# Kernel tuning notes

Hardware: AMD Instinct MI355X
Metric: run time of the kernel (lower is better)

## Reference

```python
import jax, jax.numpy as jnp
import numpy as np

N = 50000      # nodes
E = 800000     # edges (avg degree 16)
IN = 512       # in_feats
HID = 64       # hidden_dim
HEADS = 4      # num_heads
NC = 40        # num_classes


def setup_inputs() -> dict:
    key = jax.random.key(0)
    ks = jax.random.split(key, 12)

    def p(k, shape, fan_in):
        return jax.random.normal(k, shape, jnp.float32) * (1.0 / np.sqrt(fan_in))

    x = jax.random.normal(ks[0], (N, IN), jnp.float32)
    edge_index = jax.random.randint(ks[1], (2, E), 0, N)
    return dict(
        x=x,
        edge_index=edge_index,
        W1=p(ks[2], (IN, HEADS * HID), IN),
        att_src1=p(ks[3], (HEADS, HID), HID),
        att_dst1=p(ks[4], (HEADS, HID), HID),
        b1=jnp.zeros((HEADS * HID,), jnp.float32),
        W2=p(ks[5], (HEADS * HID, HID), HEADS * HID),
        att_src2=p(ks[6], (1, HID), HID),
        att_dst2=p(ks[7], (1, HID), HID),
        b2=jnp.zeros((HID,), jnp.float32),
        mw1=p(ks[8], (HID, 64), HID),
        mb1=jnp.zeros((64,), jnp.float32),
        mw2=p(ks[9], (64, NC), 64),
        mb2=jnp.zeros((NC,), jnp.float32),
    )


def gat_layer(x, edge_index, W, att_src, att_dst, bias):
    # PyG GATConv with add_self_loops=False, concat=True, negative_slope=0.2
    H, C = att_src.shape
    n = x.shape[0]
    h = (x @ W).reshape(n, H, C)                       # [N,H,C]
    a_src = jnp.sum(h * att_src, axis=-1)              # [N,H]
    a_dst = jnp.sum(h * att_dst, axis=-1)              # [N,H]
    src, dst = edge_index[0], edge_index[1]
    e = jax.nn.leaky_relu(a_src[src] + a_dst[dst], 0.2)  # [E,H]
    # segment softmax grouped by destination node
    m = jax.ops.segment_max(e, dst, num_segments=n)
    ex = jnp.exp(e - m[dst])
    denom = jax.ops.segment_sum(ex, dst, num_segments=n)
    alpha = ex / (denom[dst] + 1e-16)                  # [E,H]
    out = jax.ops.segment_sum(h[src] * alpha[:, :, None], dst, num_segments=n)  # [N,H,C]
    return out.reshape(n, H * C) + bias


def reference(x, edge_index, W1, att_src1, att_dst1, b1,
              W2, att_src2, att_dst2, b2, mw1, mb1, mw2, mb2):
    h = jax.nn.elu(gat_layer(x, edge_index, W1, att_src1, att_dst1, b1))   # [N, HEADS*HID]
    emb = gat_layer(h, edge_index, W2, att_src2, att_dst2, b2)             # [N, HID] (heads=1)
    return jax.nn.relu(emb @ mw1 + mb1) @ mw2 + mb2                        # [N, NC]
```

## Files before the change

### kernel.cpp

```cpp
#include <hip/hip_runtime.h>

#define N_NODES 50000
#define N_EDGES 800000
#define SCAN_B 196

typedef short bf16x8 __attribute__((ext_vector_type(8)));
typedef float f32x4 __attribute__((ext_vector_type(4)));

#define GLDS16(g, l)                                                  \
  __builtin_amdgcn_global_load_lds(                                   \
      (const __attribute__((address_space(1))) void*)(g),             \
      (__attribute__((address_space(3))) void*)(l), 16, 0, 0)

__device__ __forceinline__ unsigned short f2bf_rne(float x) {
  unsigned u = __float_as_uint(x);
  u += 0x7FFFu + ((u >> 16) & 1u);
  return (unsigned short)(u >> 16);
}

__device__ __forceinline__ void split2(float x, short& hi, short& lo) {
  unsigned u = __float_as_uint(x);
  unsigned short h = (unsigned short)(u >> 16);
  float hf = __uint_as_float((unsigned)h << 16);
  float r = x - hf;
  unsigned short l = (unsigned short)(__float_as_uint(r) >> 16);
  hi = (short)h;
  lo = (short)l;
}

__global__ __launch_bounds__(256) void hist_k(const int* __restrict__ ei,
                                              int* __restrict__ cnt) {
  int e = blockIdx.x * 256 + threadIdx.x;
  if (e >= N_EDGES) return;
  atomicAdd(&cnt[ei[N_EDGES + e]], 1);
}

__global__ __launch_bounds__(256) void scan1(const int* __restrict__ cnt,
                                             int* __restrict__ offs,
                                             int* __restrict__ bsum) {
  __shared__ int sh[256];
  int t = threadIdx.x;
  int i = blockIdx.x * 256 + t;
  int v = (i < N_NODES) ? cnt[i] : 0;
  sh[t] = v;
  __syncthreads();
  for (int off = 1; off < 256; off <<= 1) {
    int add = (t >= off) ? sh[t - off] : 0;
    __syncthreads();
    sh[t] += add;
    __syncthreads();
  }
  if (i < N_NODES) offs[i] = sh[t] - v;
  if (t == 255) bsum[blockIdx.x] = sh[255];
}

__global__ __launch_bounds__(256) void scan2(const int* __restrict__ bsum,
                                             int* __restrict__ bofs) {
  __shared__ int sh[256];
  int t = threadIdx.x;
  int v = (t < SCAN_B) ? bsum[t] : 0;
  sh[t] = v;
  __syncthreads();
  for (int off = 1; off < 256; off <<= 1) {
    int add = (t >= off) ? sh[t - off] : 0;
    __syncthreads();
    sh[t] += add;
    __syncthreads();
  }
  if (t < SCAN_B) bofs[t] = sh[t] - v;
}

__global__ __launch_bounds__(256) void scan3(int* __restrict__ offs,
                                             const int* __restrict__ bofs) {
  int i = blockIdx.x * 256 + threadIdx.x;
  if (i < N_NODES) offs[i] += bofs[blockIdx.x];
  if (i == 0) offs[N_NODES] = N_EDGES;
}

__global__ __launch_bounds__(256) void scatter_k(const int* __restrict__ ei,
                                                 const int* __restrict__ offs,
                                                 int* __restrict__ cur,
                                                 int* __restrict__ ssort) {
  int e = blockIdx.x * 256 + threadIdx.x;
  if (e >= N_EDGES) return;
  int d = ei[N_EDGES + e];
  int p = offs[d] + atomicAdd(&cur[d], 1);
  ssort[p] = ei[e];
}

__global__ __launch_bounds__(256) void wsplit(
    const float* __restrict__ W, unsigned short* __restrict__ Wh,
    unsigned short* __restrict__ Wl, int K, int Nn) {
  int i = blockIdx.x * 256 + threadIdx.x;
  int total = (K >> 3) * Nn;
  if (i >= total) return;
  int kq = i / Nn;
  int n = i % Nn;
  alignas(16) short h[8], l[8];
#pragma unroll
  for (int j = 0; j < 8; ++j) {
    float v = W[(size_t)(kq * 8 + j) * Nn + n];
    split2(v, h[j], l[j]);
  }
  size_t dst = (size_t)i * 8;
  *(bf16x8*)&Wh[dst] = *(bf16x8*)h;
  *(bf16x8*)&Wl[dst] = *(bf16x8*)l;
}

__global__ __launch_bounds__(256) void gemm1_fused(
    const float* __restrict__ A,
    const unsigned short* __restrict__ Bh_g, const unsigned short* __restrict__ Bl_g,
    const float* __restrict__ att_s, const float* __restrict__ att_d,
    unsigned short* __restrict__ h1b, float* __restrict__ asrc,
    float* __restrict__ adst, int M) {
  constexpr int K = 512, Nn = 256;
  constexpr int LDA = 40;
  __shared__ short Ah[128][LDA], Al[128][LDA];
  __shared__ short Bh[4 * 128 * 8], Bl[4 * 128 * 8];
  __shared__ float attLds[128][4];

  const int tid = threadIdx.x;
  const int wave = tid >> 6, lane = tid & 63;
  const int quad = lane >> 4, l16 = lane & 15;
  const int wm = (wave >> 1) * 64, wn = (wave & 1) * 64;
  const int rowBase = blockIdx.x * 128;
  const int colBase = blockIdx.y * 128;

  const int ra = tid >> 1, apart = (tid & 1) * 16;
  const int arow = min(rowBase + ra, M - 1);
  const float* aptr = A + (size_t)arow * K + apart;

  f32x4 acc[4][4] = {};

  for (int kc = 0; kc < K / 32; ++kc) {
#pragma unroll
    for (int inst = 0; inst < 2; ++inst) {
      int seq = inst * 256 + tid;
      int gq = seq >> 7, nl = seq & 127;
      size_t gsrc = (((size_t)kc * 4 + gq) * Nn + colBase + nl) * 8;
      GLDS16(Bh_g + gsrc, &Bh[seq * 8]);
      GLDS16(Bl_g + gsrc, &Bl[seq * 8]);
    }
    {
      alignas(16) short h[16], l[16];
      const float4* a4 = (const float4*)(aptr + kc * 32);
#pragma unroll
      for (int i = 0; i < 4; ++i) {
        float4 v = a4[i];
        split2(v.x, h[i * 4 + 0], l[i * 4 + 0]);
        split2(v.y, h[i * 4 + 1], l[i * 4 + 1]);
        split2(v.z, h[i * 4 + 2], l[i * 4 + 2]);
        split2(v.w, h[i * 4 + 3], l[i * 4 + 3]);
      }
      *(bf16x8*)&Ah[ra][apart]     = ((bf16x8*)h)[0];
      *(bf16x8*)&Ah[ra][apart + 8] = ((bf16x8*)h)[1];
      *(bf16x8*)&Al[ra][apart]     = ((bf16x8*)l)[0];
      *(bf16x8*)&Al[ra][apart + 8] = ((bf16x8*)l)[1];
    }
    __syncthreads();
    bf16x8 afh[4], afl[4], bfh[4], bfl[4];
#pragma unroll
    for (int mt = 0; mt < 4; ++mt) {
      afh[mt] = *(const bf16x8*)&Ah[wm + mt * 16 + l16][quad * 8];
      afl[mt] = *(const bf16x8*)&Al[wm + mt * 16 + l16][quad * 8];
    }
#pragma unroll
    for (int nt = 0; nt < 4; ++nt) {
      int bi = ((quad << 7) + wn + nt * 16 + l16) * 8;
      bfh[nt] = *(const bf16x8*)&Bh[bi];
      bfl[nt] = *(const bf16x8*)&Bl[bi];
    }
#pragma unroll
    for (int mt = 0; mt < 4; ++mt)
#pragma unroll
      for (int nt = 0; nt < 4; ++nt) {
        acc[mt][nt] = __builtin_amdgcn_mfma_f32_16x16x32_bf16(afh[mt], bfh[nt], acc[mt][nt], 0, 0, 0);
        acc[mt][nt] = __builtin_amdgcn_mfma_f32_16x16x32_bf16(afh[mt], bfl[nt], acc[mt][nt], 0, 0, 0);
        acc[mt][nt] = __builtin_amdgcn_mfma_f32_16x16x32_bf16(afl[mt], bfh[nt], acc[mt][nt], 0, 0, 0);
      }
    __syncthreads();
  }

  float asw[4], adw[4];
#pragma unroll
  for (int nt = 0; nt < 4; ++nt) {
    int c = colBase + wn + nt * 16 + l16;
    asw[nt] = att_s[c];
    adw[nt] = att_d[c];
  }
#pragma unroll
  for (int mt = 0; mt < 4; ++mt) {
    int rl = wm + mt * 16 + quad * 4;
#pragma unroll
    for (int reg = 0; reg < 4; ++reg) {
      int r = rowBase + rl + reg;
      float s = 0.f, dd = 0.f;
#pragma unroll
      for (int nt = 0; nt < 4; ++nt) {
        float v = acc[mt][nt][reg];
        s += v * asw[nt];
        dd += v * adw[nt];
        if (r < M) {
          int c = colBase + wn + nt * 16 + l16;
          h1b[(size_t)r * Nn + c] = f2bf_rne(v);
        }
      }
#pragma unroll
      for (int off = 1; off < 16; off <<= 1) {
        s += __shfl_xor(s, off);
        dd += __shfl_xor(dd, off);
      }
      if (l16 == 0) {
        attLds[rl + reg][(wn >> 6) * 2 + 0] = s;
        attLds[rl + reg][(wn >> 6) * 2 + 1] = dd;
      }
    }
  }
  __syncthreads();
  if (tid < 128) {
    int r = rowBase + tid;
    if (r < M) {
      int hb = colBase >> 6;
      asrc[r * 4 + hb + 0] = attLds[tid][0];
      adst[r * 4 + hb + 0] = attLds[tid][1];
      asrc[r * 4 + hb + 1] = attLds[tid][2];
      adst[r * 4 + hb + 1] = attLds[tid][3];
    }
  }
}

__global__ __launch_bounds__(256) void gemm2_fused(
    const float* __restrict__ A,
    const unsigned short* __restrict__ Bh_g, const unsigned short* __restrict__ Bl_g,
    const float* __restrict__ att_s, const float* __restrict__ att_d,
    unsigned short* __restrict__ h2b, float* __restrict__ asrc,
    float* __restrict__ adst, int M) {
  constexpr int K = 256, Nn = 64;
  constexpr int LDA = 40;
  __shared__ short Ah[128][LDA], Al[128][LDA];
  __shared__ short Bh[4 * 64 * 8], Bl[4 * 64 * 8];
  __shared__ float attLds[128][2];

  const int tid = threadIdx.x;
  const int wave = tid >> 6, lane = tid & 63;
  const int quad = lane >> 4, l16 = lane & 15;
  const int wm = wave * 32;
  const int rowBase = blockIdx.x * 128;

  const int ra = tid >> 1, apart = (tid & 1) * 16;
  const int arow = min(rowBase + ra, M - 1);
  const float* aptr = A + (size_t)arow * K + apart;

  f32x4 acc[2][4] = {};

  for (int kc = 0; kc < K / 32; ++kc) {
    {
      size_t gsrc = (((size_t)kc * 4) * Nn) * 8 + (size_t)tid * 8;
      GLDS16(Bh_g + gsrc, &Bh[tid * 8]);
      GLDS16(Bl_g + gsrc, &Bl[tid * 8]);
    }
    {
      alignas(16) short h[16], l[16];
      const float4* a4 = (const float4*)(aptr + kc * 32);
#pragma unroll
      for (int i = 0; i < 4; ++i) {
        float4 v = a4[i];
        split2(v.x, h[i * 4 + 0], l[i * 4 + 0]);
        split2(v.y, h[i * 4 + 1], l[i * 4 + 1]);
        split2(v.z, h[i * 4 + 2], l[i * 4 + 2]);
        split2(v.w, h[i * 4 + 3], l[i * 4 + 3]);
      }
      *(bf16x8*)&Ah[ra][apart]     = ((bf16x8*)h)[0];
      *(bf16x8*)&Ah[ra][apart + 8] = ((bf16x8*)h)[1];
      *(bf16x8*)&Al[ra][apart]     = ((bf16x8*)l)[0];
      *(bf16x8*)&Al[ra][apart + 8] = ((bf16x8*)l)[1];
    }
    __syncthreads();
    bf16x8 afh[2], afl[2], bfh[4], bfl[4];
#pragma unroll
    for (int mt = 0; mt < 2; ++mt) {
      afh[mt] = *(const bf16x8*)&Ah[wm + mt * 16 + l16][quad * 8];
      afl[mt] = *(const bf16x8*)&Al[wm + mt * 16 + l16][quad * 8];
    }
#pragma unroll
    for (int nt = 0; nt < 4; ++nt) {
      int bi = ((quad << 6) + nt * 16 + l16) * 8;
      bfh[nt] = *(const bf16x8*)&Bh[bi];
      bfl[nt] = *(const bf16x8*)&Bl[bi];
    }
#pragma unroll
    for (int mt = 0; mt < 2; ++mt)
#pragma unroll
      for (int nt = 0; nt < 4; ++nt) {
        acc[mt][nt] = __builtin_amdgcn_mfma_f32_16x16x32_bf16(afh[mt], bfh[nt], acc[mt][nt], 0, 0, 0);
        acc[mt][nt] = __builtin_amdgcn_mfma_f32_16x16x32_bf16(afh[mt], bfl[nt], acc[mt][nt], 0, 0, 0);
        acc[mt][nt] = __builtin_amdgcn_mfma_f32_16x16x32_bf16(afl[mt], bfh[nt], acc[mt][nt], 0, 0, 0);
      }
    __syncthreads();
  }

  float asw[4], adw[4];
#pragma unroll
  for (int nt = 0; nt < 4; ++nt) {
    int c = nt * 16 + l16;
    asw[nt] = att_s[c];
    adw[nt] = att_d[c];
  }
#pragma unroll
  for (int mt = 0; mt < 2; ++mt) {
    int rl = wm + mt * 16 + quad * 4;
#pragma unroll
    for (int reg = 0; reg < 4; ++reg) {
      int r = rowBase + rl + reg;
      float s = 0.f, dd = 0.f;
#pragma unroll
      for (int nt = 0; nt < 4; ++nt) {
        float v = acc[mt][nt][reg];
        s += v * asw[nt];
        dd += v * adw[nt];
        if (r < M) {
          int c = nt * 16 + l16;
          h2b[(size_t)r * Nn + c] = f2bf_rne(v);
        }
      }
#pragma unroll
      for (int off = 1; off < 16; off <<= 1) {
        s += __shfl_xor(s, off);
        dd += __shfl_xor(dd, off);
      }
      if (l16 == 0) {
        attLds[rl + reg][0] = s;
        attLds[rl + reg][1] = dd;
      }
    }
  }
  __syncthreads();
  if (tid < 128) {
    int r = rowBase + tid;
    if (r < M) {
      asrc[r] = attLds[tid][0];
      adst[r] = attLds[tid][1];
    }
  }
}

__global__ __launch_bounds__(128) void agg_l1(
    const int* __restrict__ offs, const int* __restrict__ ssort,
    const float* __restrict__ asrc, const float* __restrict__ adst,
    const unsigned short* __restrict__ h1b, const float* __restrict__ b1,
    float* __restrict__ outp) {
  const int d = blockIdx.x;
  const int t = threadIdx.x;
  const int h = t >> 5;
  __shared__ int s_src[128];
  __shared__ float s_ex[128 * 4];
  const int row0 = offs[d], row1 = offs[d + 1];
  const float4 ad4 = *(const float4*)&adst[d * 4];
  float acc0 = 0.f, acc1 = 0.f, denom = 0.f;

  for (int j0 = row0; j0 < row1; j0 += 128) {
    const int n = min(128, row1 - j0);
    if (t < n) {
      int s = ssort[j0 + t];
      s_src[t] = s;
      float4 as = *(const float4*)&asrc[s * 4];
      float4 sc;
      sc.x = as.x + ad4.x; sc.x = sc.x > 0.f ? sc.x : 0.2f * sc.x;
      sc.y = as.y + ad4.y; sc.y = sc.y > 0.f ? sc.y : 0.2f * sc.y;
      sc.z = as.z + ad4.z; sc.z = sc.z > 0.f ? sc.z : 0.2f * sc.z;
      sc.w = as.w + ad4.w; sc.w = sc.w > 0.f ? sc.w : 0.2f * sc.w;
      sc.x = __expf(sc.x); sc.y = __expf(sc.y);
      sc.z = __expf(sc.z); sc.w = __expf(sc.w);
      *(float4*)&s_ex[t * 4] = sc;
    }
    __syncthreads();
    for (int j = 0; j < n; ++j) {
      float exv = s_ex[j * 4 + h];
      unsigned pv = *(const unsigned*)&h1b[(size_t)s_src[j] * 256 + 2 * t];
      float f0 = __uint_as_float(pv << 16);
      float f1 = __uint_as_float(pv & 0xFFFF0000u);
      acc0 += f0 * exv;
      acc1 += f1 * exv;
      denom += exv;
    }
    __syncthreads();
  }
  float inv = denom > 0.f ? 1.f / denom : 0.f;
  float v0 = acc0 * inv + b1[2 * t];
  float v1 = acc1 * inv + b1[2 * t + 1];
  float2 r;
  r.x = v0 > 0.f ? v0 : expm1f(v0);
  r.y = v1 > 0.f ? v1 : expm1f(v1);
  *(float2*)&outp[(size_t)d * 256 + 2 * t] = r;
}

__global__ __launch_bounds__(256) void agg_l2(
    const int* __restrict__ offs, const int* __restrict__ ssort,
    const float* __restrict__ asrc, const float* __restrict__ adst,
    const unsigned short* __restrict__ h2b, const float* __restrict__ b2,
    float* __restrict__ outp, int n_nodes) {
  int d = blockIdx.x * 4 + (threadIdx.x >> 6);
  int lane = threadIdx.x & 63;
  if (d >= n_nodes) return;
  const int row0 = offs[d], row1 = offs[d + 1];
  const float ad = adst[d];
  float acc = 0.f, denom = 0.f;

  for (int j0 = row0; j0 < row1; j0 += 64) {
    const int n = min(64, row1 - j0);
    int s = 0;
    float ex = 0.f;
    if (lane < n) {
      s = ssort[j0 + lane];
      float sc = asrc[s] + ad;
      sc = sc > 0.f ? sc : 0.2f * sc;
      ex = __expf(sc);
    }
    float ds = ex;
#pragma unroll
    for (int off = 32; off > 0; off >>= 1) ds += __shfl_xor(ds, off);
    denom += ds;
    for (int j = 0; j < n; ++j) {
      int sj = __shfl(s, j);
      float exj = __shfl(ex, j);
      float f = __uint_as_float((unsigned)h2b[(size_t)sj * 64 + lane] << 16);
      acc += f * exj;
    }
  }
  float val = (denom > 0.f ? acc / denom : 0.f) + b2[lane];
  outp[(size_t)d * 64 + lane] = val;
}

__global__ __launch_bounds__(256) void mlp_head(
    const float* __restrict__ emb_in,
    const float* __restrict__ mw1, const float* __restrict__ mb1,
    const float* __restrict__ mw2, const float* __restrict__ mb2,
    float* __restrict__ outp, int n) {
  __shared__ float w1s[64 * 64];
  __shared__ float w2s[64 * 40];
  __shared__ float b1s[64];
  __shared__ float b2s[40];
  int t = threadIdx.x;
  for (int i = t; i < 64 * 64; i += 256) w1s[i] = mw1[i];
  for (int i = t; i < 64 * 40; i += 256) w2s[i] = mw2[i];
  if (t < 64) b1s[t] = mb1[t];
  if (t < 40) b2s[t] = mb2[t];
  __syncthreads();
  int node = blockIdx.x * 256 + t;
  if (node >= n) return;
  float emb[64];
#pragma unroll
  for (int i = 0; i < 64; ++i) emb[i] = emb_in[(size_t)node * 64 + i];
  float hid[64];
#pragma unroll
  for (int j = 0; j < 64; ++j) {
    float s = b1s[j];
#pragma unroll
    for (int i = 0; i < 64; ++i) s += emb[i] * w1s[i * 64 + j];
    hid[j] = s > 0.f ? s : 0.f;
  }
#pragma unroll
  for (int k = 0; k < 40; ++k) {
    float s = b2s[k];
#pragma unroll
    for (int j = 0; j < 64; ++j) s += hid[j] * w2s[j * 40 + k];
    outp[(size_t)node * 40 + k] = s;
  }
}

extern "C" void kernel_launch(void* const* d_in, const int* in_sizes, int n_in,
                              void* d_out, int out_size, void* d_ws, size_t ws_size,
                              hipStream_t stream) {
  const float* x        = (const float*)d_in[0];
  const int*   ei       = (const int*)d_in[1];
  const float* W1       = (const float*)d_in[2];
  const float* att_src1 = (const float*)d_in[3];
  const float* att_dst1 = (const float*)d_in[4];
  const float* b1       = (const float*)d_in[5];
  const float* W2       = (const float*)d_in[6];
  const float* att_src2 = (const float*)d_in[7];
  const float* att_dst2 = (const float*)d_in[8];
  const float* b2       = (const float*)d_in[9];
  const float* mw1      = (const float*)d_in[10];
  const float* mb1      = (const float*)d_in[11];
  const float* mw2      = (const float*)d_in[12];
  const float* mb2      = (const float*)d_in[13];
  float* out = (float*)d_out;

  const int N = N_NODES, E = N_EDGES;
  char* base = (char*)d_ws;
  size_t o = 0;
  auto alloc = [&](size_t n_elems) {
    void* p = base + o;
    o += n_elems * 4;
    return p;
  };
  int* cnt = (int*)alloc(N);
  int* cur = (int*)alloc(N);
  size_t zero_bytes = o;
  int*   offs  = (int*)alloc(N + 2);
  int*   bsum  = (int*)alloc(256);
  int*   bofs  = (int*)alloc(256);
  int*   ssort = (int*)alloc(E);
  float* h1e   = (float*)alloc((size_t)N * 256);
  float* asrc1 = (float*)alloc((size_t)N * 4);
  float* adst1 = (float*)alloc((size_t)N * 4);
  float* emb   = (float*)alloc((size_t)N * 64);
  float* asrc2 = (float*)alloc(N);
  float* adst2 = (float*)alloc(N);
  unsigned short* h1b = (unsigned short*)alloc((size_t)N * 128);
  unsigned short* h2b = (unsigned short*)alloc((size_t)N * 32);
  unsigned short* w1h = (unsigned short*)alloc(512 * 256 / 2);
  unsigned short* w1l = (unsigned short*)alloc(512 * 256 / 2);
  unsigned short* w2h = (unsigned short*)alloc(256 * 64 / 2);
  unsigned short* w2l = (unsigned short*)alloc(256 * 64 / 2);

  hipMemsetAsync(d_ws, 0, zero_bytes, stream);

  const int EB = (E + 255) / 256;

  hist_k<<<EB, 256, 0, stream>>>(ei, cnt);
  scan1<<<SCAN_B, 256, 0, stream>>>(cnt, offs, bsum);
  scan2<<<1, 256, 0, stream>>>(bsum, bofs);
  scan3<<<SCAN_B, 256, 0, stream>>>(offs, bofs);
  scatter_k<<<EB, 256, 0, stream>>>(ei, offs, cur, ssort);
  wsplit<<<(512 / 8 * 256 + 255) / 256, 256, 0, stream>>>(W1, w1h, w1l, 512, 256);
  wsplit<<<(256 / 8 * 64 + 255) / 256, 256, 0, stream>>>(W2, w2h, w2l, 256, 64);

  dim3 g1((N + 127) / 128, 2);
  gemm1_fused<<<g1, 256, 0, stream>>>(x, w1h, w1l, att_src1, att_dst1,
                                      h1b, asrc1, adst1, N);
  agg_l1<<<N, 128, 0, stream>>>(offs, ssort, asrc1, adst1, h1b, b1, h1e);

  dim3 g2((N + 127) / 128, 1);
  gemm2_fused<<<g2, 256, 0, stream>>>(h1e, w2h, w2l, att_src2, att_dst2,
                                      h2b, asrc2, adst2, N);
  agg_l2<<<(N + 3) / 4, 256, 0, stream>>>(offs, ssort, asrc2, adst2, h2b, b2, emb, N);

  mlp_head<<<(N + 255) / 256, 256, 0, stream>>>(emb, mw1, mb1, mw2, mb2, out, N);
}
```

Before: 514.8 us.

## Double-buffer LDS tiles in both GEMM kernels to overlap loads with MFMA

```diff
diff --git a/kernel.cpp b/kernel.cpp
--- a/kernel.cpp
+++ b/kernel.cpp
@@ -113,10 +113,10 @@
     const float* __restrict__ att_s, const float* __restrict__ att_d,
     unsigned short* __restrict__ h1b, float* __restrict__ asrc,
     float* __restrict__ adst, int M) {
-  constexpr int K = 512, Nn = 256;
+  constexpr int K = 512, Nn = 256, NKC = K / 32;
   constexpr int LDA = 40;
-  __shared__ short Ah[128][LDA], Al[128][LDA];
-  __shared__ short Bh[4 * 128 * 8], Bl[4 * 128 * 8];
+  __shared__ short Ah[2][128][LDA], Al[2][128][LDA];
+  __shared__ short Bh[2][4 * 128 * 8], Bl[2][4 * 128 * 8];
   __shared__ float attLds[128][4];
 
   const int tid = threadIdx.x;
@@ -132,43 +132,60 @@
 
   f32x4 acc[4][4] = {};
 
-  for (int kc = 0; kc < K / 32; ++kc) {
-#pragma unroll
-    for (int inst = 0; inst < 2; ++inst) {
-      int seq = inst * 256 + tid;
-      int gq = seq >> 7, nl = seq & 127;
-      size_t gsrc = (((size_t)kc * 4 + gq) * Nn + colBase + nl) * 8;
-      GLDS16(Bh_g + gsrc, &Bh[seq * 8]);
-      GLDS16(Bl_g + gsrc, &Bl[seq * 8]);
-    }
-    {
-      alignas(16) short h[16], l[16];
-      const float4* a4 = (const float4*)(aptr + kc * 32);
-#pragma unroll
-      for (int i = 0; i < 4; ++i) {
-        float4 v = a4[i];
-        split2(v.x, h[i * 4 + 0], l[i * 4 + 0]);
-        split2(v.y, h[i * 4 + 1], l[i * 4 + 1]);
-        split2(v.z, h[i * 4 + 2], l[i * 4 + 2]);
-        split2(v.w, h[i * 4 + 3], l[i * 4 + 3]);
-      }
-      *(bf16x8*)&Ah[ra][apart]     = ((bf16x8*)h)[0];
-      *(bf16x8*)&Ah[ra][apart + 8] = ((bf16x8*)h)[1];
-      *(bf16x8*)&Al[ra][apart]     = ((bf16x8*)l)[0];
-      *(bf16x8*)&Al[ra][apart + 8] = ((bf16x8*)l)[1];
-    }
-    __syncthreads();
+#pragma unroll
+  for (int inst = 0; inst < 2; ++inst) {
+    int seq = inst * 256 + tid;
+    int gq = seq >> 7, nl = seq & 127;
+    size_t gsrc = (((size_t)gq) * Nn + colBase + nl) * 8;
+    GLDS16(Bh_g + gsrc, &Bh[0][seq * 8]);
+    GLDS16(Bl_g + gsrc, &Bl[0][seq * 8]);
+  }
+  {
+    alignas(16) short h[16], l[16];
+    const float4* a4 = (const float4*)(aptr);
+#pragma unroll
+    for (int i = 0; i < 4; ++i) {
+      float4 v = a4[i];
+      split2(v.x, h[i * 4 + 0], l[i * 4 + 0]);
+      split2(v.y, h[i * 4 + 1], l[i * 4 + 1]);
+      split2(v.z, h[i * 4 + 2], l[i * 4 + 2]);
+      split2(v.w, h[i * 4 + 3], l[i * 4 + 3]);
+    }
+    *(bf16x8*)&Ah[0][ra][apart]     = ((bf16x8*)h)[0];
+    *(bf16x8*)&Ah[0][ra][apart + 8] = ((bf16x8*)h)[1];
+    *(bf16x8*)&Al[0][ra][apart]     = ((bf16x8*)l)[0];
+    *(bf16x8*)&Al[0][ra][apart + 8] = ((bf16x8*)l)[1];
+  }
+  __syncthreads();
+
+  for (int kc = 0; kc < NKC; ++kc) {
+    const int cur = kc & 1, nxt = cur ^ 1;
+    const bool hasNext = (kc + 1 < NKC);
+    float4 av[4];
+    if (hasNext) {
+#pragma unroll
+      for (int inst = 0; inst < 2; ++inst) {
+        int seq = inst * 256 + tid;
+        int gq = seq >> 7, nl = seq & 127;
+        size_t gsrc = (((size_t)(kc + 1) * 4 + gq) * Nn + colBase + nl) * 8;
+        GLDS16(Bh_g + gsrc, &Bh[nxt][seq * 8]);
+        GLDS16(Bl_g + gsrc, &Bl[nxt][seq * 8]);
+      }
+      const float4* a4 = (const float4*)(aptr + (kc + 1) * 32);
+#pragma unroll
+      for (int i = 0; i < 4; ++i) av[i] = a4[i];
+    }
     bf16x8 afh[4], afl[4], bfh[4], bfl[4];
 #pragma unroll
     for (int mt = 0; mt < 4; ++mt) {
-      afh[mt] = *(const bf16x8*)&Ah[wm + mt * 16 + l16][quad * 8];
-      afl[mt] = *(const bf16x8*)&Al[wm + mt * 16 + l16][quad * 8];
+      afh[mt] = *(const bf16x8*)&Ah[cur][wm + mt * 16 + l16][quad * 8];
+      afl[mt] = *(const bf16x8*)&Al[cur][wm + mt * 16 + l16][quad * 8];
     }
 #pragma unroll
     for (int nt = 0; nt < 4; ++nt) {
       int bi = ((quad << 7) + wn + nt * 16 + l16) * 8;
-      bfh[nt] = *(const bf16x8*)&Bh[bi];
-      bfl[nt] = *(const bf16x8*)&Bl[bi];
+      bfh[nt] = *(const bf16x8*)&Bh[cur][bi];
+      bfl[nt] = *(const bf16x8*)&Bl[cur][bi];
     }
 #pragma unroll
     for (int mt = 0; mt < 4; ++mt)
@@ -178,6 +195,21 @@
         acc[mt][nt] = __builtin_amdgcn_mfma_f32_16x16x32_bf16(afh[mt], bfl[nt], acc[mt][nt], 0, 0, 0);
         acc[mt][nt] = __builtin_amdgcn_mfma_f32_16x16x32_bf16(afl[mt], bfh[nt], acc[mt][nt], 0, 0, 0);
       }
+    __builtin_amdgcn_sched_barrier(0);
+    if (hasNext) {
+      alignas(16) short h[16], l[16];
+#pragma unroll
+      for (int i = 0; i < 4; ++i) {
+        split2(av[i].x, h[i * 4 + 0], l[i * 4 + 0]);
+        split2(av[i].y, h[i * 4 + 1], l[i * 4 + 1]);
+        split2(av[i].z, h[i * 4 + 2], l[i * 4 + 2]);
+        split2(av[i].w, h[i * 4 + 3], l[i * 4 + 3]);
+      }
+      *(bf16x8*)&Ah[nxt][ra][apart]     = ((bf16x8*)h)[0];
+      *(bf16x8*)&Ah[nxt][ra][apart + 8] = ((bf16x8*)h)[1];
+      *(bf16x8*)&Al[nxt][ra][apart]     = ((bf16x8*)l)[0];
+      *(bf16x8*)&Al[nxt][ra][apart + 8] = ((bf16x8*)l)[1];
+    }
     __syncthreads();
   }
 
@@ -235,10 +267,10 @@
     const float* __restrict__ att_s, const float* __restrict__ att_d,
     unsigned short* __restrict__ h2b, float* __restrict__ asrc,
     float* __restrict__ adst, int M) {
-  constexpr int K = 256, Nn = 64;
+  constexpr int K = 256, Nn = 64, NKC = K / 32;
   constexpr int LDA = 40;
-  __shared__ short Ah[128][LDA], Al[128][LDA];
-  __shared__ short Bh[4 * 64 * 8], Bl[4 * 64 * 8];
+  __shared__ short Ah[2][128][LDA], Al[2][128][LDA];
+  __shared__ short Bh[2][4 * 64 * 8], Bl[2][4 * 64 * 8];
   __shared__ float attLds[128][2];
 
   const int tid = threadIdx.x;
@@ -253,40 +285,54 @@
 
   f32x4 acc[2][4] = {};
 
-  for (int kc = 0; kc < K / 32; ++kc) {
-    {
-      size_t gsrc = (((size_t)kc * 4) * Nn) * 8 + (size_t)tid * 8;
-      GLDS16(Bh_g + gsrc, &Bh[tid * 8]);
-      GLDS16(Bl_g + gsrc, &Bl[tid * 8]);
-    }
-    {
-      alignas(16) short h[16], l[16];
-      const float4* a4 = (const float4*)(aptr + kc * 32);
-#pragma unroll
-      for (int i = 0; i < 4; ++i) {
-        float4 v = a4[i];
-        split2(v.x, h[i * 4 + 0], l[i * 4 + 0]);
-        split2(v.y, h[i * 4 + 1], l[i * 4 + 1]);
-        split2(v.z, h[i * 4 + 2], l[i * 4 + 2]);
-        split2(v.w, h[i * 4 + 3], l[i * 4 + 3]);
-      }
-      *(bf16x8*)&Ah[ra][apart]     = ((bf16x8*)h)[0];
-      *(bf16x8*)&Ah[ra][apart + 8] = ((bf16x8*)h)[1];
-      *(bf16x8*)&Al[ra][apart]     = ((bf16x8*)l)[0];
-      *(bf16x8*)&Al[ra][apart + 8] = ((bf16x8*)l)[1];
-    }
-    __syncthreads();
+  {
+    size_t gsrc = (size_t)tid * 8;
+    GLDS16(Bh_g + gsrc, &Bh[0][tid * 8]);
+    GLDS16(Bl_g + gsrc, &Bl[0][tid * 8]);
+  }
+  {
+    alignas(16) short h[16], l[16];
+    const float4* a4 = (const float4*)(aptr);
+#pragma unroll
+    for (int i = 0; i < 4; ++i) {
+      float4 v = a4[i];
+      split2(v.x, h[i * 4 + 0], l[i * 4 + 0]);
+      split2(v.y, h[i * 4 + 1], l[i * 4 + 1]);
+      split2(v.z, h[i * 4 + 2], l[i * 4 + 2]);
+      split2(v.w, h[i * 4 + 3], l[i * 4 + 3]);
+    }
+    *(bf16x8*)&Ah[0][ra][apart]     = ((bf16x8*)h)[0];
+    *(bf16x8*)&Ah[0][ra][apart + 8] = ((bf16x8*)h)[1];
+    *(bf16x8*)&Al[0][ra][apart]     = ((bf16x8*)l)[0];
+    *(bf16x8*)&Al[0][ra][apart + 8] = ((bf16x8*)l)[1];
+  }
+  __syncthreads();
+
+  for (int kc = 0; kc < NKC; ++kc) {
+    const int cur = kc & 1, nxt = cur ^ 1;
+    const bool hasNext = (kc + 1 < NKC);
+    float4 av[4];
+    if (hasNext) {
+      {
+        size_t gsrc = (((size_t)(kc + 1) * 4) * Nn) * 8 + (size_t)tid * 8;
+        GLDS16(Bh_g + gsrc, &Bh[nxt][tid * 8]);
+        GLDS16(Bl_g + gsrc, &Bl[nxt][tid * 8]);
+      }
+      const float4* a4 = (const float4*)(aptr + (kc + 1) * 32);
+#pragma unroll
+      for (int i = 0; i < 4; ++i) av[i] = a4[i];
+    }
     bf16x8 afh[2], afl[2], bfh[4], bfl[4];
 #pragma unroll
     for (int mt = 0; mt < 2; ++mt) {
-      afh[mt] = *(const bf16x8*)&Ah[wm + mt * 16 + l16][quad * 8];
-      afl[mt] = *(const bf16x8*)&Al[wm + mt * 16 + l16][quad * 8];
+      afh[mt] = *(const bf16x8*)&Ah[cur][wm + mt * 16 + l16][quad * 8];
+      afl[mt] = *(const bf16x8*)&Al[cur][wm + mt * 16 + l16][quad * 8];
     }
 #pragma unroll
     for (int nt = 0; nt < 4; ++nt) {
       int bi = ((quad << 6) + nt * 16 + l16) * 8;
-      bfh[nt] = *(const bf16x8*)&Bh[bi];
-      bfl[nt] = *(const bf16x8*)&Bl[bi];
+      bfh[nt] = *(const bf16x8*)&Bh[cur][bi];
+      bfl[nt] = *(const bf16x8*)&Bl[cur][bi];
     }
 #pragma unroll
     for (int mt = 0; mt < 2; ++mt)
@@ -296,6 +342,21 @@
         acc[mt][nt] = __builtin_amdgcn_mfma_f32_16x16x32_bf16(afh[mt], bfl[nt], acc[mt][nt], 0, 0, 0);
         acc[mt][nt] = __builtin_amdgcn_mfma_f32_16x16x32_bf16(afl[mt], bfh[nt], acc[mt][nt], 0, 0, 0);
       }
+    __builtin_amdgcn_sched_barrier(0);
+    if (hasNext) {
+      alignas(16) short h[16], l[16];
+#pragma unroll
+      for (int i = 0; i < 4; ++i) {
+        split2(av[i].x, h[i * 4 + 0], l[i * 4 + 0]);
+        split2(av[i].y, h[i * 4 + 1], l[i * 4 + 1]);
+        split2(av[i].z, h[i * 4 + 2], l[i * 4 + 2]);
+        split2(av[i].w, h[i * 4 + 3], l[i * 4 + 3]);
+      }
+      *(bf16x8*)&Ah[nxt][ra][apart]     = ((bf16x8*)h)[0];
+      *(bf16x8*)&Ah[nxt][ra][apart + 8] = ((bf16x8*)h)[1];
+      *(bf16x8*)&Al[nxt][ra][apart]     = ((bf16x8*)l)[0];
+      *(bf16x8*)&Al[nxt][ra][apart + 8] = ((bf16x8*)l)[1];
+    }
     __syncthreads();
   }
 
```

After: 528.2 us. +2.6%, slower.

## Process multiple edges in parallel with vectorized bf16 gathers in GAT aggregation

Applied to the files above, without the earlier changes.

```diff
diff --git a/kernel.cpp b/kernel.cpp
--- a/kernel.cpp
+++ b/kernel.cpp
@@ -5,6 +5,7 @@
 #define SCAN_B 196
 
 typedef short bf16x8 __attribute__((ext_vector_type(8)));
+typedef short bf16x4 __attribute__((ext_vector_type(4)));
 typedef float f32x4 __attribute__((ext_vector_type(4)));
 
 #define GLDS16(g, l)                                                  \
@@ -351,15 +352,18 @@
     float* __restrict__ outp) {
   const int d = blockIdx.x;
   const int t = threadIdx.x;
-  const int h = t >> 5;
-  __shared__ int s_src[128];
-  __shared__ float s_ex[128 * 4];
+  const int g = t >> 5, lt = t & 31;
+  const int h = lt >> 3;
+  __shared__ int s_src[32];
+  __shared__ float s_ex[32 * 4];
+  __shared__ float red[4][32][9];
   const int row0 = offs[d], row1 = offs[d + 1];
   const float4 ad4 = *(const float4*)&adst[d * 4];
-  float acc0 = 0.f, acc1 = 0.f, denom = 0.f;
-
-  for (int j0 = row0; j0 < row1; j0 += 128) {
-    const int n = min(128, row1 - j0);
+  float acc[8] = {};
+  float denom = 0.f;
+
+  for (int j0 = row0; j0 < row1; j0 += 32) {
+    const int n = min(32, row1 - j0);
     if (t < n) {
       int s = ssort[j0 + t];
       s_src[t] = s;
@@ -374,24 +378,41 @@
       *(float4*)&s_ex[t * 4] = sc;
     }
     __syncthreads();
-    for (int j = 0; j < n; ++j) {
-      float exv = s_ex[j * 4 + h];
-      unsigned pv = *(const unsigned*)&h1b[(size_t)s_src[j] * 256 + 2 * t];
-      float f0 = __uint_as_float(pv << 16);
-      float f1 = __uint_as_float(pv & 0xFFFF0000u);
-      acc0 += f0 * exv;
-      acc1 += f1 * exv;
+    for (int jj = g; jj < n; jj += 4) {
+      int s = s_src[jj];
+      float exv = s_ex[jj * 4 + h];
+      bf16x8 pv = *(const bf16x8*)&h1b[(size_t)s * 256 + lt * 8];
+#pragma unroll
+      for (int k = 0; k < 8; ++k) {
+        float f = __uint_as_float((unsigned)(unsigned short)pv[k] << 16);
+        acc[k] += f * exv;
+      }
       denom += exv;
     }
     __syncthreads();
   }
-  float inv = denom > 0.f ? 1.f / denom : 0.f;
-  float v0 = acc0 * inv + b1[2 * t];
-  float v1 = acc1 * inv + b1[2 * t + 1];
-  float2 r;
-  r.x = v0 > 0.f ? v0 : expm1f(v0);
-  r.y = v1 > 0.f ? v1 : expm1f(v1);
-  *(float2*)&outp[(size_t)d * 256 + 2 * t] = r;
+#pragma unroll
+  for (int k = 0; k < 8; ++k) red[g][lt][k] = acc[k];
+  red[g][lt][8] = denom;
+  __syncthreads();
+  if (g == 0) {
+    float a[8], dn;
+    dn = red[0][lt][8] + red[1][lt][8] + red[2][lt][8] + red[3][lt][8];
+#pragma unroll
+    for (int k = 0; k < 8; ++k)
+      a[k] = red[0][lt][k] + red[1][lt][k] + red[2][lt][k] + red[3][lt][k];
+    float inv = dn > 0.f ? 1.f / dn : 0.f;
+    float o[8];
+#pragma unroll
+    for (int k = 0; k < 8; ++k) {
+      float v = a[k] * inv + b1[lt * 8 + k];
+      o[k] = v > 0.f ? v : expm1f(v);
+    }
+    float4 r0 = {o[0], o[1], o[2], o[3]};
+    float4 r1 = {o[4], o[5], o[6], o[7]};
+    *(float4*)&outp[(size_t)d * 256 + lt * 8]     = r0;
+    *(float4*)&outp[(size_t)d * 256 + lt * 8 + 4] = r1;
+  }
 }
 
 __global__ __launch_bounds__(256) void agg_l2(
@@ -402,33 +423,46 @@
   int d = blockIdx.x * 4 + (threadIdx.x >> 6);
   int lane = threadIdx.x & 63;
   if (d >= n_nodes) return;
+  const int eg = lane >> 4, fl = lane & 15;
   const int row0 = offs[d], row1 = offs[d + 1];
   const float ad = adst[d];
-  float acc = 0.f, denom = 0.f;
-
-  for (int j0 = row0; j0 < row1; j0 += 64) {
-    const int n = min(64, row1 - j0);
+  float acc[4] = {};
+  float denom = 0.f;
+
+  for (int j0 = row0; j0 < row1; j0 += 4) {
+    int jm = j0 + eg;
     int s = 0;
     float ex = 0.f;
-    if (lane < n) {
-      s = ssort[j0 + lane];
+    if (jm < row1) {
+      s = ssort[jm];
       float sc = asrc[s] + ad;
       sc = sc > 0.f ? sc : 0.2f * sc;
       ex = __expf(sc);
     }
-    float ds = ex;
-#pragma unroll
-    for (int off = 32; off > 0; off >>= 1) ds += __shfl_xor(ds, off);
-    denom += ds;
-    for (int j = 0; j < n; ++j) {
-      int sj = __shfl(s, j);
-      float exj = __shfl(ex, j);
-      float f = __uint_as_float((unsigned)h2b[(size_t)sj * 64 + lane] << 16);
-      acc += f * exj;
-    }
-  }
-  float val = (denom > 0.f ? acc / denom : 0.f) + b2[lane];
-  outp[(size_t)d * 64 + lane] = val;
+    bf16x4 pv = *(const bf16x4*)&h2b[(size_t)s * 64 + fl * 4];
+#pragma unroll
+    for (int k = 0; k < 4; ++k) {
+      float f = __uint_as_float((unsigned)(unsigned short)pv[k] << 16);
+      acc[k] += f * ex;
+    }
+    denom += ex;
+  }
+#pragma unroll
+  for (int k = 0; k < 4; ++k) {
+    acc[k] += __shfl_xor(acc[k], 16);
+    acc[k] += __shfl_xor(acc[k], 32);
+  }
+  denom += __shfl_xor(denom, 16);
+  denom += __shfl_xor(denom, 32);
+  float inv = denom > 0.f ? 1.f / denom : 0.f;
+  if (eg == 0) {
+    float4 r;
+    r.x = acc[0] * inv + b2[fl * 4 + 0];
+    r.y = acc[1] * inv + b2[fl * 4 + 1];
+    r.z = acc[2] * inv + b2[fl * 4 + 2];
+    r.w = acc[3] * inv + b2[fl * 4 + 3];
+    *(float4*)&outp[(size_t)d * 64 + fl * 4] = r;
+  }
 }
 
 __global__ __launch_bounds__(256) void mlp_head(
@@ -492,7 +526,7 @@
   size_t o = 0;
   auto alloc = [&](size_t n_elems) {
     void* p = base + o;
-    o += n_elems * 4;
+    o = (o + n_elems * 4 + 15) & ~(size_t)15;
     return p;
   };
   int* cnt = (int*)alloc(N);
```

Result: no change. 516.5 us (+0.3%).
